# Optimization experiments

Measured on AMD Instinct MI355X. Metric: run time of the kernel, lower is better.

Reference implementation:

```python
import jax, jax.numpy as jnp
import numpy as np

# Dimensions (match init_kwargs / input_specs)
N, F, E = 50000, 256, 200000   # nodes, in-features, edges
H, C = 4, 128                  # heads, per-head channels (hidden_dim)
G, NC = 256, 10                # graphs in batch, num_classes
EPS = 1e-16                    # PyG softmax denominator epsilon


def _lin(key, fin, fout):
    kw, kb = jax.random.split(key)
    W = jax.random.normal(kw, (fin, fout), jnp.float32) / np.float32(np.sqrt(fin))
    b = jax.random.normal(kb, (fout,), jnp.float32) * 0.01
    return W, b


def setup_inputs() -> dict:
    key = jax.random.key(0)
    ks = jax.random.split(key, 16)
    x = jax.random.normal(ks[0], (N, F), jnp.float32)
    edge_index = jax.random.randint(ks[1], (2, E), 0, N)
    batch = jnp.sort(jax.random.randint(ks[2], (N,), 0, G))
    d = {"x": x, "edge_index": edge_index, "batch": batch}
    # layer1: in=F, out=H*C (concat=True); layer2: in=H*C, out=C (concat=False, skip -> C)
    d["Wq1"], d["bq1"] = _lin(ks[3], F, H * C)
    d["Wk1"], d["bk1"] = _lin(ks[4], F, H * C)
    d["Wv1"], d["bv1"] = _lin(ks[5], F, H * C)
    d["Ws1"], d["bs1"] = _lin(ks[6], F, H * C)
    d["Wq2"], d["bq2"] = _lin(ks[7], H * C, H * C)
    d["Wk2"], d["bk2"] = _lin(ks[8], H * C, H * C)
    d["Wv2"], d["bv2"] = _lin(ks[9], H * C, H * C)
    d["Ws2"], d["bs2"] = _lin(ks[10], H * C, C)
    d["Wfc"], d["bfc"] = _lin(ks[11], C, NC)
    return d


def _tconv(x, src, dst, Wq, bq, Wk, bk, Wv, bv, Ws, bs, concat):
    """PyG TransformerConv (root_weight=True, beta=False), eval mode (no dropout)."""
    n = x.shape[0]
    q = (x @ Wq + bq).reshape(n, H, C)
    k = (x @ Wk + bk).reshape(n, H, C)
    v = (x @ Wv + bv).reshape(n, H, C)
    # per-edge scores: query from dst node i, key/value from src node j
    alpha = jnp.einsum('ehc,ehc->eh', q[dst], k[src]) / jnp.float32(np.sqrt(C))  # [E,H]
    m = jax.ops.segment_max(alpha, dst, num_segments=n)          # [N,H]
    e = jnp.exp(alpha - m[dst])                                  # [E,H]
    s = jax.ops.segment_sum(e, dst, num_segments=n)              # [N,H]
    a = e / (s[dst] + EPS)                                       # segment softmax over dst
    msg = jax.ops.segment_sum(a[:, :, None] * v[src], dst, num_segments=n)  # [N,H,C]
    out = msg.reshape(n, H * C) if concat else msg.mean(axis=1)
    return out + x @ Ws + bs  # root/skip connection


def reference(x, edge_index, batch,
              Wq1, bq1, Wk1, bk1, Wv1, bv1, Ws1, bs1,
              Wq2, bq2, Wk2, bk2, Wv2, bv2, Ws2, bs2,
              Wfc, bfc):
    src, dst = edge_index[0], edge_index[1]
    h = jax.nn.elu(_tconv(x, src, dst, Wq1, bq1, Wk1, bk1, Wv1, bv1, Ws1, bs1, True))
    # dropout is identity in eval mode
    h = jax.nn.elu(_tconv(h, src, dst, Wq2, bq2, Wk2, bk2, Wv2, bv2, Ws2, bs2, False))
    cnt = jax.ops.segment_sum(jnp.ones((h.shape[0],), h.dtype), batch, num_segments=G)
    pooled = jax.ops.segment_sum(h, batch, num_segments=G) / jnp.maximum(cnt, 1.0)[:, None]
    return jax.nn.log_softmax(pooled @ Wfc + bfc, axis=1)  # [G, NC]
```

## Files before the change

### kernel.cpp

```cpp
#include <hip/hip_runtime.h>
#include <math.h>
#include <stdint.h>

#define N_NODES 50000
#define FEAT    256
#define EDGES   200000
#define HEADS   4
#define CH      128
#define HID     512
#define NGRAPH  256
#define NCLS    10

typedef unsigned short ushort_t;
typedef unsigned int uint_t;
typedef __attribute__((ext_vector_type(8))) short bf16x8;
typedef __attribute__((ext_vector_type(4))) float f32x4;
typedef __attribute__((ext_vector_type(2))) float f32x2;

__device__ __forceinline__ ushort_t f2bf(float f) {
  uint_t u = __float_as_uint(f);
  u += 0x7FFF + ((u >> 16) & 1);
  return (ushort_t)(u >> 16);
}
__device__ __forceinline__ float bf2f(ushort_t h) {
  return __uint_as_float(((uint_t)h) << 16);
}
__device__ __forceinline__ float elu1(float x) {
  return x > 0.f ? x : __expf(x) - 1.f;
}
__device__ __forceinline__ float fastrcp(float x) {
  return __builtin_amdgcn_rcpf(x);
}
__device__ __forceinline__ void unpack8(uint4 w, float* f) {
  f[0] = bf2f((ushort_t)w.x); f[1] = bf2f((ushort_t)(w.x >> 16));
  f[2] = bf2f((ushort_t)w.y); f[3] = bf2f((ushort_t)(w.y >> 16));
  f[4] = bf2f((ushort_t)w.z); f[5] = bf2f((ushort_t)(w.z >> 16));
  f[6] = bf2f((ushort_t)w.w); f[7] = bf2f((ushort_t)(w.w >> 16));
}
__device__ __forceinline__ void unpack8_fp8(uint2 w, float* f) {
  f32x2 a = __builtin_amdgcn_cvt_pk_f32_fp8((int)w.x, false);
  f32x2 b = __builtin_amdgcn_cvt_pk_f32_fp8((int)w.x, true);
  f32x2 c = __builtin_amdgcn_cvt_pk_f32_fp8((int)w.y, false);
  f32x2 d = __builtin_amdgcn_cvt_pk_f32_fp8((int)w.y, true);
  f[0] = a[0]; f[1] = a[1]; f[2] = b[0]; f[3] = b[1];
  f[4] = c[0]; f[5] = c[1]; f[6] = d[0]; f[7] = d[1];
}
__device__ __forceinline__ uint_t pack4_fp8(float f0, float f1, float f2, float f3) {
  int v = __builtin_amdgcn_cvt_pk_fp8_f32(f0, f1, 0, false);
  v = __builtin_amdgcn_cvt_pk_fp8_f32(f2, f3, v, true);
  return (uint_t)v;
}


__global__ __launch_bounds__(256) void gemm_bt(
    const ushort_t* __restrict__ A, const ushort_t* __restrict__ Bt,
    const float* __restrict__ bias, char* __restrict__ Cb,
    char* __restrict__ Cb2, int M, int K, int nct, int mode) {
  __shared__ __align__(16) ushort_t smem[24576];
  const int tid = threadIdx.x;
  const int lane = tid & 63, wave = tid >> 6;
  const int wr = wave >> 1, wc = wave & 1;

  int b = blockIdx.x;
  int per = nct << 3;
  int grp = b / per;
  int rem = b - grp * per;
  int rloc = rem & 7;
  int ct = rem >> 3;
  const int rowBase = (grp * 8 + rloc) * 128;
  const int colBase = ct * 128;
  if (rowBase >= M) return;

  const int s0 = tid, s1 = tid + 256;
  const int rl0 = s0 >> 2, cg0 = (s0 & 3) ^ ((rl0 >> 1) & 3);
  const int rl1 = s1 >> 2, cg1 = (s1 & 3) ^ ((rl1 >> 1) & 3);
  int ra0 = rowBase + rl0; ra0 = ra0 < M ? ra0 : M - 1;
  int ra1 = rowBase + rl1; ra1 = ra1 < M ? ra1 : M - 1;
  const ushort_t* pa0 = A + (size_t)ra0 * K + cg0 * 8;
  const ushort_t* pa1 = A + (size_t)ra1 * K + cg1 * 8;
  const ushort_t* pb0 = Bt + (size_t)(colBase + rl0) * K + cg0 * 8;
  const ushort_t* pb1 = Bt + (size_t)(colBase + rl1) * K + cg1 * 8;
  const int dA0 = s0 * 8, dA1 = s1 * 8;
  const int dB0 = 4096 + s0 * 8, dB1 = 4096 + s1 * 8;

#define GLL(gp, loff)  __builtin_amdgcn_global_load_lds( \
      (const __attribute__((address_space(1))) uint_t*)(gp), \
      (__attribute__((address_space(3))) uint_t*)(smem + (loff)), 16, 0, 0)

  const int nt = K >> 5;
  GLL(pa0, dA0);            GLL(pa1, dA1);
  GLL(pb0, dB0);            GLL(pb1, dB1);
  GLL(pa0 + 32, 8192 + dA0); GLL(pa1 + 32, 8192 + dA1);
  GLL(pb0 + 32, 8192 + dB0); GLL(pb1 + 32, 8192 + dB1);
  pa0 += 64; pa1 += 64; pb0 += 64; pb1 += 64;

  const int fr = lane & 15, c0 = lane >> 4;
  const int pswz = (c0 ^ ((fr >> 1) & 3)) * 8;
  const int aOff = (wr * 64 + fr) * 32 + pswz;
  const int bOff = 4096 + (wc * 64 + fr) * 32 + pswz;

  f32x4 acc[4][4] = {};
  asm volatile("s_waitcnt vmcnt(4)" ::: "memory");
  __builtin_amdgcn_s_barrier();
  __builtin_amdgcn_sched_barrier(0);

  int cur = 0, nxt = 2;
  for (int t = 0; t < nt; ++t) {
    const ushort_t* bufc = smem + cur * 8192;
    const bool pf = (t + 2) < nt;
    bf16x8 af[4], bfr[4];
    af[0] = *(const bf16x8*)(bufc + aOff);
#pragma unroll
    for (int j = 0; j < 4; ++j) bfr[j] = *(const bf16x8*)(bufc + bOff + j * 512);
#pragma unroll
    for (int i = 1; i < 4; ++i) af[i] = *(const bf16x8*)(bufc + aOff + i * 512);
    if (pf) {
      int lo = nxt * 8192;
      GLL(pa0, lo + dA0); GLL(pa1, lo + dA1);
      GLL(pb0, lo + dB0); GLL(pb1, lo + dB1);
      pa0 += 32; pa1 += 32; pb0 += 32; pb1 += 32;
    }
#pragma unroll
    for (int i = 0; i < 4; ++i)
#pragma unroll
      for (int j = 0; j < 4; ++j)
        acc[i][j] = __builtin_amdgcn_mfma_f32_16x16x32_bf16(af[i], bfr[j], acc[i][j], 0, 0, 0);
    asm volatile("s_waitcnt lgkmcnt(0)" ::: "memory");
    if (pf)                asm volatile("s_waitcnt vmcnt(4)" ::: "memory");
    else if (t + 1 < nt)   asm volatile("s_waitcnt vmcnt(0)" ::: "memory");
    __builtin_amdgcn_s_barrier();
    __builtin_amdgcn_sched_barrier(0);
    cur = cur == 2 ? 0 : cur + 1;
    nxt = nxt == 2 ? 0 : nxt + 1;
  }
#undef GLL

  char* obase; int ostride, koff, isfp8;
  if (mode == 1) {
    int H = colBase >> 9, sel = (colBase >> 7) & 3;
    if (sel == 0)      { obase = Cb;  ostride = 2304; koff = H * 256; isfp8 = 0; }
    else if (sel == 3) { obase = Cb2; ostride = 1024; koff = H * 256; isfp8 = 0; }
    else { obase = Cb; ostride = 2304;
           koff = 1024 + H * 256 + (sel == 2 ? 8 : 0); isfp8 = 1; }
  } else {
    obase = Cb; ostride = 2304;
    if (colBase == 768) { koff = 2048; isfp8 = 0; }
    else {
      int n2 = (colBase < 768) ? colBase : colBase - 896;
      int hb = (colBase < 768) ? 0 : 2;
      int hh = hb + n2 / 384, r = n2 % 384, sel = r >> 7;
      if (sel == 0) { koff = hh * 256; isfp8 = 0; }
      else          { koff = 1024 + hh * 256 + (sel == 2 ? 8 : 0); isfp8 = 1; }
    }
  }

  ushort_t* wbuf = smem + wave * 2048;
  const int rq = lane >> 4, fc = lane & 15;
  float bv[4];
#pragma unroll
  for (int j = 0; j < 4; ++j) bv[j] = bias[colBase + wc * 64 + j * 16 + fc];
#pragma unroll
  for (int h = 0; h < 2; ++h) {
#pragma unroll
    for (int ii = 0; ii < 2; ++ii) {
      int i = h * 2 + ii;
#pragma unroll
      for (int j = 0; j < 4; ++j)
#pragma unroll
        for (int r = 0; r < 4; ++r) {
          int rl = ii * 16 + rq * 4 + r;
          int cl = j * 16 + fc;
          int cs = cl ^ (rq << 4);
          wbuf[rl * 64 + cs] = f2bf(acc[i][j][r] + bv[j]);
        }
    }
    int ci = lane & 7;
    int rbase = lane >> 3;
#pragma unroll
    for (int rg = 0; rg < 4; ++rg) {
      int rr = rg * 8 + rbase;
      int rowg = rowBase + wr * 64 + h * 32 + rr;
      int cg = ci ^ (((rr >> 2) & 3) << 1);
      uint4 val = *(const uint4*)(wbuf + rr * 64 + (ci << 3));
      if (rowg < M) {
        char* dstRow = obase + (size_t)rowg * ostride + koff;
        if (!isfp8) {
          *(uint4*)(dstRow + (wc * 64 + cg * 8) * 2) = val;
        } else {
          float f[8];
          f[0] = bf2f((ushort_t)val.x); f[1] = bf2f((ushort_t)(val.x >> 16));
          f[2] = bf2f((ushort_t)val.y); f[3] = bf2f((ushort_t)(val.y >> 16));
          f[4] = bf2f((ushort_t)val.z); f[5] = bf2f((ushort_t)(val.z >> 16));
          f[6] = bf2f((ushort_t)val.w); f[7] = bf2f((ushort_t)(val.w >> 16));
          uint2 o;
          o.x = pack4_fp8(f[0], f[1], f[2], f[3]);
          o.y = pack4_fp8(f[4], f[5], f[6], f[7]);
          *(uint2*)(dstRow + ((wc * 8 + cg) << 4)) = o;
        }
      }
    }
  }
}

#define L1_W   (2048 * FEAT)
#define L2_W   (1664 * HID)
#define T1     512
#define T2     832
#define NB_CVT  12500
#define NB_TP   (T1 + T2)
#define NB_BIAS 15
#define NB_ZERO 196

__global__ __launch_bounds__(256) void prep_all(
    const float* __restrict__ x, ushort_t* __restrict__ xb,
    const float* __restrict__ Wq1, const float* __restrict__ Wk1,
    const float* __restrict__ Wv1, const float* __restrict__ Ws1,
    const float* __restrict__ Wq2, const float* __restrict__ Wk2,
    const float* __restrict__ Wv2, const float* __restrict__ Ws2,
    const float* __restrict__ bq1, const float* __restrict__ bk1,
    const float* __restrict__ bv1, const float* __restrict__ bs1,
    const float* __restrict__ bq2, const float* __restrict__ bk2,
    const float* __restrict__ bv2, const float* __restrict__ bs2,
    ushort_t* __restrict__ W1t, ushort_t* __restrict__ W2t,
    float* __restrict__ Bh1, float* __restrict__ Bh2,
    int* __restrict__ deg, int* __restrict__ counter,
    int* __restrict__ gstart, int* __restrict__ gend) {
  __shared__ float tile[32][33];
  int blk = blockIdx.x;
  if (blk < NB_CVT) {
    int i = blk * 256 + threadIdx.x;
    float4 f = *(const float4*)(x + (size_t)i * 4);
    uint_t lo = (uint_t)f2bf(f.x) | ((uint_t)f2bf(f.y) << 16);
    uint_t hi = (uint_t)f2bf(f.z) | ((uint_t)f2bf(f.w) << 16);
    ((uint2*)xb)[i] = make_uint2(lo, hi);
    return;
  }
  blk -= NB_CVT;
  if (blk < NB_TP) {
    int t = blk;
    const float* W; int ldw, c0, n0, k0, ldk; ushort_t* dst;
    if (t < T1) {
      int nb = t >> 3, kb = t & 7;
      n0 = nb * 32; k0 = kb * 32; ldk = FEAT; dst = W1t;
      int p = n0 >> 10, n1 = n0 & 1023, hh = n1 >> 9, sel = (n1 >> 7) & 3;
      c0 = (2 * p + hh) * CH + (n1 & (CH - 1));
      W = sel == 0 ? Wq1 : sel == 1 ? Wk1 : sel == 2 ? Wv1 : Ws1;
      ldw = HID;
    } else {
      t -= T1;
      int nb = t >> 4, kb = t & 15;
      n0 = nb * 32; k0 = kb * 32; ldk = HID; dst = W2t;
      if (n0 < 768 || n0 >= 896) {
        int n2 = (n0 < 768) ? n0 : n0 - 896;
        int hb = (n0 < 768) ? 0 : 2;
        int hh = hb + n2 / 384, r = n2 % 384, sel = r >> 7;
        c0 = hh * CH + (r & (CH - 1));
        W = sel == 0 ? Wq2 : sel == 1 ? Wk2 : Wv2;
        ldw = HID;
      } else {
        c0 = n0 - 768; W = Ws2; ldw = CH;
      }
    }
    int col = threadIdx.x & 31, rw = threadIdx.x >> 5;
#pragma unroll
    for (int ph = 0; ph < 4; ++ph) {
      int kk = rw + ph * 8;
      tile[kk][col] = W[(size_t)(k0 + kk) * ldw + c0 + col];
    }
    __syncthreads();
#pragma unroll
    for (int ph = 0; ph < 4; ++ph) {
      int dn = rw + ph * 8;
      dst[(size_t)(n0 + dn) * ldk + k0 + col] = f2bf(tile[col][dn]);
    }
    return;
  }
  blk -= NB_TP;
  if (blk < NB_BIAS) {
    int n = blk * 256 + threadIdx.x;
    if (n < 2048) {
      int p = n >> 10, n1 = n & 1023, hh = n1 >> 9, sel = (n1 >> 7) & 3;
      int c = (2 * p + hh) * CH + (n1 & (CH - 1));
      const float* bb = sel == 0 ? bq1 : sel == 1 ? bk1 : sel == 2 ? bv1 : bs1;
      Bh1[n] = bb[c];
    } else if (n < 2048 + 1664) {
      int n2 = n - 2048;
      if (n2 < 768 || n2 >= 896) {
        int nn = (n2 < 768) ? n2 : n2 - 896;
        int hb = (n2 < 768) ? 0 : 2;
        int hh = hb + nn / 384, r = nn % 384, sel = r >> 7;
        int c = hh * CH + (r & (CH - 1));
        const float* bb = sel == 0 ? bq2 : sel == 1 ? bk2 : bv2;
        Bh2[n2] = bb[c];
      } else {
        Bh2[n2] = bs2[n2 - 768];
      }
    }
    return;
  }
  blk -= NB_BIAS;
  {
    int i = blk * 256 + threadIdx.x;
    if (i < N_NODES) deg[i] = 0;
    if (i < NGRAPH) { gstart[i] = 0; gend[i] = 0; }
    if (i == 0) counter[0] = 0;
  }
}

__global__ void hist_bounds_kernel(const int* __restrict__ dst, int* __restrict__ deg,
                                   const int* __restrict__ batch,
                                   int* __restrict__ gstart, int* __restrict__ gend) {
  int t = blockIdx.x * blockDim.x + threadIdx.x;
  if (t < EDGES) atomicAdd(&deg[dst[t]], 1);
  if (t < N_NODES) {
    int b = batch[t];
    if (t == 0 || batch[t - 1] != b) gstart[b] = t;
    if (t == N_NODES - 1 || batch[t + 1] != b) gend[b] = t + 1;
  }
}

__global__ void alloc_kernel(const int* __restrict__ deg, int* __restrict__ counter,
                             int* __restrict__ start, int* __restrict__ cursor) {
  int i = blockIdx.x * blockDim.x + threadIdx.x;
  int lane = threadIdx.x & 63;
  int v = (i < N_NODES) ? deg[i] : 0;
  int sum = v;
#pragma unroll
  for (int off = 1; off < 64; off <<= 1) {
    int t = __shfl_up(sum, off);
    if (lane >= off) sum += t;
  }
  int excl = sum - v;
  int waveTot = __shfl(sum, 63);
  int base = 0;
  if (lane == 63) base = atomicAdd(counter, waveTot);
  base = __shfl(base, 63);
  if (i < N_NODES) {
    start[i] = base + excl;
    cursor[i] = base + excl;
  }
}

__global__ void scatter_kernel(const int* __restrict__ src, const int* __restrict__ dst,
                               int* __restrict__ cursor, int* __restrict__ csr) {
  int e = blockIdx.x * blockDim.x + threadIdx.x;
  if (e < EDGES) {
    int pos = atomicAdd(&cursor[dst[e]], 1);
    csr[pos] = src[e];
  }
}

#define INV_SQRT_CH 0.08838834764831845f

__global__ __launch_bounds__(256) void attn1_kernel(
    const char* __restrict__ BIG, const int* __restrict__ start,
    const int* __restrict__ deg, const int* __restrict__ csr,
    ushort_t* __restrict__ H1b) {
  int wave = threadIdx.x >> 6, lane = threadIdx.x & 63;
  int li = lane & 15, g = lane >> 4;
  int i = blockIdx.x * 4 + wave;
  if (i >= N_NODES) return;
  int beg = start[i], end = beg + deg[i];
  const int kvoff = 1024 + g * 256 + li * 16;
  float q[8];
  unpack8(*(const uint4*)(BIG + (size_t)i * 2304 + g * 256 + li * 16), q);
  float s = 0.f, a[8] = {};
  if (beg < end) {
    int j = csr[beg];
    uint4 kv = *(const uint4*)(BIG + (size_t)j * 2304 + kvoff);
    for (int e = beg; e < end; ++e) {
      int en = e + 1 < end ? e + 1 : e;
      int jn = csr[en];
      uint4 kvn = *(const uint4*)(BIG + (size_t)jn * 2304 + kvoff);
      float kf[8];
      unpack8_fp8(make_uint2(kv.x, kv.y), kf);
      float pd = q[0]*kf[0]+q[1]*kf[1]+q[2]*kf[2]+q[3]*kf[3]+
                 q[4]*kf[4]+q[5]*kf[5]+q[6]*kf[6]+q[7]*kf[7];
      pd += __shfl_xor(pd, 1);
      pd += __shfl_xor(pd, 2);
      pd += __shfl_xor(pd, 4);
      pd += __shfl_xor(pd, 8);
      float w = __expf(pd * INV_SQRT_CH);
      float vf[8];
      unpack8_fp8(make_uint2(kv.z, kv.w), vf);
      s += w;
#pragma unroll
      for (int c = 0; c < 8; ++c) a[c] = fmaf(w, vf[c], a[c]);
      kv = kvn;
    }
  }
  float inv = fastrcp(s + 1e-16f);
  ushort_t* op8 = H1b + (size_t)i * HID + g * CH + li * 8;
  float sk[8];
  unpack8(*(const uint4*)op8, sk);
  uint4 ow;
  uint_t* op = (uint_t*)&ow;
#pragma unroll
  for (int c = 0; c < 4; ++c) {
    float o0 = elu1(a[2 * c] * inv + sk[2 * c]);
    float o1 = elu1(a[2 * c + 1] * inv + sk[2 * c + 1]);
    op[c] = (uint_t)f2bf(o0) | ((uint_t)f2bf(o1) << 16);
  }
  *(uint4*)op8 = ow;
}

__global__ __launch_bounds__(256) void attn2_kernel(
    const char* __restrict__ BIG, const int* __restrict__ start,
    const int* __restrict__ deg, const int* __restrict__ csr,
    ushort_t* __restrict__ POut) {
  int wave = threadIdx.x >> 6, lane = threadIdx.x & 63;
  int li = lane & 15, g = lane >> 4;
  int i = blockIdx.x * 4 + wave;
  if (i >= N_NODES) return;
  int beg = start[i], end = beg + deg[i];
  const int kvoff = 1024 + g * 256 + li * 16;
  float q[8];
  unpack8(*(const uint4*)(BIG + (size_t)i * 2304 + g * 256 + li * 16), q);
  float s = 0.f, a[8] = {};
  if (beg < end) {
    int j = csr[beg];
    uint4 kv = *(const uint4*)(BIG + (size_t)j * 2304 + kvoff);
    for (int e = beg; e < end; ++e) {
      int en = e + 1 < end ? e + 1 : e;
      int jn = csr[en];
      uint4 kvn = *(const uint4*)(BIG + (size_t)jn * 2304 + kvoff);
      float kf[8];
      unpack8_fp8(make_uint2(kv.x, kv.y), kf);
      float pd = q[0]*kf[0]+q[1]*kf[1]+q[2]*kf[2]+q[3]*kf[3]+
                 q[4]*kf[4]+q[5]*kf[5]+q[6]*kf[6]+q[7]*kf[7];
      pd += __shfl_xor(pd, 1);
      pd += __shfl_xor(pd, 2);
      pd += __shfl_xor(pd, 4);
      pd += __shfl_xor(pd, 8);
      float w = __expf(pd * INV_SQRT_CH);
      float vf[8];
      unpack8_fp8(make_uint2(kv.z, kv.w), vf);
      s += w;
#pragma unroll
      for (int c = 0; c < 8; ++c) a[c] = fmaf(w, vf[c], a[c]);
      kv = kvn;
    }
  }
  float inv = 0.25f * fastrcp(s + 1e-16f);
  float o[8];
#pragma unroll
  for (int c = 0; c < 8; ++c) o[c] = a[c] * inv;
#pragma unroll
  for (int ox = 16; ox <= 32; ox <<= 1)
#pragma unroll
    for (int c = 0; c < 8; ++c) o[c] += __shfl_xor(o[c], ox);
  if (g != 0) return;
  uint4 ow;
  uint_t* op = (uint_t*)&ow;
#pragma unroll
  for (int c = 0; c < 4; ++c)
    op[c] = (uint_t)f2bf(o[2 * c]) | ((uint_t)f2bf(o[2 * c + 1]) << 16);
  *(uint4*)(POut + (size_t)i * CH + li * 8) = ow;
}

__global__ __launch_bounds__(256) void pool_cls(
    const ushort_t* __restrict__ POut, const char* __restrict__ BIG,
    const int* __restrict__ gstart, const int* __restrict__ gend,
    const float* __restrict__ Wfc, const float* __restrict__ bfc,
    float* __restrict__ out) {
  int g = blockIdx.x;
  int t = threadIdx.x;
  int c = t & (CH - 1), rr = t >> 7;
  int s0 = gstart[g], e0 = gend[g];
  float sum = 0.f;
  for (int i = s0 + rr; i < e0; i += 2) {
    float sk = bf2f(*(const ushort_t*)(BIG + (size_t)i * 2304 + 2048 + c * 2));
    float m0 = bf2f(POut[(size_t)i * CH + c]);
    sum += elu1(sk + m0);
  }
  __shared__ float sh[256];
  __shared__ float p[CH];
  __shared__ float red[CH];
  __shared__ float logits[NCLS];
  sh[t] = sum;
  __syncthreads();
  if (t < CH) {
    float cnt = fmaxf((float)(e0 - s0), 1.f);
    p[t] = (sh[t] + sh[t + CH]) / cnt;
  }
  for (int cc = 0; cc < NCLS; ++cc) {
    __syncthreads();
    if (t < CH) red[t] = p[t] * Wfc[t * NCLS + cc];
    __syncthreads();
    for (int off = 64; off > 0; off >>= 1) {
      if (t < off) red[t] += red[t + off];
      __syncthreads();
    }
    if (t == 0) logits[cc] = red[0] + bfc[cc];
  }
  __syncthreads();
  if (t == 0) {
    float mx = -INFINITY;
    for (int cc = 0; cc < NCLS; ++cc) mx = fmaxf(mx, logits[cc]);
    float se = 0.f;
    for (int cc = 0; cc < NCLS; ++cc) se += expf(logits[cc] - mx);
    float ls = mx + logf(se);
    for (int cc = 0; cc < NCLS; ++cc) out[g * NCLS + cc] = logits[cc] - ls;
  }
}

extern "C" void kernel_launch(void* const* d_in, const int* in_sizes, int n_in,
                              void* d_out, int out_size, void* d_ws, size_t ws_size,
                              hipStream_t stream) {
  const float* x    = (const float*)d_in[0];
  const int*   ei   = (const int*)d_in[1];
  const int*   batch= (const int*)d_in[2];
  const float* Wq1 = (const float*)d_in[3];  const float* bq1 = (const float*)d_in[4];
  const float* Wk1 = (const float*)d_in[5];  const float* bk1 = (const float*)d_in[6];
  const float* Wv1 = (const float*)d_in[7];  const float* bv1 = (const float*)d_in[8];
  const float* Ws1 = (const float*)d_in[9];  const float* bs1 = (const float*)d_in[10];
  const float* Wq2 = (const float*)d_in[11]; const float* bq2 = (const float*)d_in[12];
  const float* Wk2 = (const float*)d_in[13]; const float* bk2 = (const float*)d_in[14];
  const float* Wv2 = (const float*)d_in[15]; const float* bv2 = (const float*)d_in[16];
  const float* Ws2 = (const float*)d_in[17]; const float* bs2 = (const float*)d_in[18];
  const float* Wfc = (const float*)d_in[19]; const float* bfc = (const float*)d_in[20];
  float* out = (float*)d_out;

  ushort_t* xb     = (ushort_t*)d_ws;
  ushort_t* POut   = (ushort_t*)d_ws;
  char*     BIG    = (char*)(xb + (size_t)N_NODES * FEAT);
  ushort_t* H1b    = (ushort_t*)(BIG + (size_t)N_NODES * 2304);
  ushort_t* W1t    = H1b + (size_t)N_NODES * HID;
  float*    Bh1    = (float*)(W1t + L1_W);
  ushort_t* W2t    = (ushort_t*)(Bh1 + 2048);
  float*    Bh2    = (float*)(W2t + L2_W);
  int* deg    = (int*)(Bh2 + 1664);
  int* start  = deg + N_NODES;
  int* cursor = start + N_NODES;
  int* csr    = cursor + N_NODES;
  int* gstart = csr + EDGES;
  int* gend   = gstart + NGRAPH;
  int* counter= gend + NGRAPH;

  const int* srcp = ei;
  const int* dstp = ei + EDGES;

  prep_all<<<NB_CVT + NB_TP + NB_BIAS + NB_ZERO, 256, 0, stream>>>(
      x, xb, Wq1, Wk1, Wv1, Ws1, Wq2, Wk2, Wv2, Ws2,
      bq1, bk1, bv1, bs1, bq2, bk2, bv2, bs2,
      W1t, W2t, Bh1, Bh2, deg, counter, gstart, gend);
  hist_bounds_kernel<<<(EDGES + 255) / 256, 256, 0, stream>>>(dstp, deg, batch, gstart, gend);
  alloc_kernel<<<(N_NODES + 255) / 256, 256, 0, stream>>>(deg, counter, start, cursor);
  scatter_kernel<<<(EDGES + 255) / 256, 256, 0, stream>>>(srcp, dstp, cursor, csr);

  const int ga = (N_NODES + 3) / 4;

  gemm_bt<<<49 * 8 * 16, 256, 0, stream>>>(
      xb, W1t, Bh1, BIG, (char*)H1b, N_NODES, FEAT, 16, 1);
  attn1_kernel<<<ga, 256, 0, stream>>>(BIG, start, deg, csr, H1b);

  gemm_bt<<<49 * 8 * 13, 256, 0, stream>>>(
      H1b, W2t, Bh2, BIG, (char*)H1b, N_NODES, HID, 13, 2);
  attn2_kernel<<<ga, 256, 0, stream>>>(BIG, start, deg, csr, POut);

  pool_cls<<<NGRAPH, 256, 0, stream>>>(POut, BIG, gstart, gend, Wfc, bfc, out);
}
```

Measured before the change: 472.6 us.

## Unroll attention edge loops by two and split pooling across chunked blocks

The attention kernels now process two edges per iteration with separate accumulators and two gathers in flight, which adds memory-level parallelism to the latency-bound neighbor gathers. Attn1 also loads the skip values before the loop rather than after it. The pooling+classifier kernel is split into a chunked partial-sum kernel (256x8 blocks with float atomics into a zeroed buffer) and a small final classifier kernel. This raises parallelism in pooling but adds one launch and makes the float summation order nondeterministic.

```diff
diff --git a/kernel.cpp b/kernel.cpp
--- a/kernel.cpp
+++ b/kernel.cpp
@@ -224,7 +224,8 @@
     ushort_t* __restrict__ W1t, ushort_t* __restrict__ W2t,
     float* __restrict__ Bh1, float* __restrict__ Bh2,
     int* __restrict__ deg, int* __restrict__ counter,
-    int* __restrict__ gstart, int* __restrict__ gend) {
+    int* __restrict__ gstart, int* __restrict__ gend,
+    float* __restrict__ pooled) {
   __shared__ float tile[32][33];
   int blk = blockIdx.x;
   if (blk < NB_CVT) {
@@ -303,6 +304,7 @@
     int i = blk * 256 + threadIdx.x;
     if (i < N_NODES) deg[i] = 0;
     if (i < NGRAPH) { gstart[i] = 0; gend[i] = 0; }
+    if (i < NGRAPH * CH) pooled[i] = 0.f;
     if (i == 0) counter[0] = 0;
   }
 }
@@ -364,41 +366,67 @@
   const int kvoff = 1024 + g * 256 + li * 16;
   float q[8];
   unpack8(*(const uint4*)(BIG + (size_t)i * 2304 + g * 256 + li * 16), q);
-  float s = 0.f, a[8] = {};
-  if (beg < end) {
-    int j = csr[beg];
-    uint4 kv = *(const uint4*)(BIG + (size_t)j * 2304 + kvoff);
-    for (int e = beg; e < end; ++e) {
-      int en = e + 1 < end ? e + 1 : e;
-      int jn = csr[en];
-      uint4 kvn = *(const uint4*)(BIG + (size_t)jn * 2304 + kvoff);
-      float kf[8];
-      unpack8_fp8(make_uint2(kv.x, kv.y), kf);
-      float pd = q[0]*kf[0]+q[1]*kf[1]+q[2]*kf[2]+q[3]*kf[3]+
-                 q[4]*kf[4]+q[5]*kf[5]+q[6]*kf[6]+q[7]*kf[7];
-      pd += __shfl_xor(pd, 1);
-      pd += __shfl_xor(pd, 2);
-      pd += __shfl_xor(pd, 4);
-      pd += __shfl_xor(pd, 8);
-      float w = __expf(pd * INV_SQRT_CH);
-      float vf[8];
-      unpack8_fp8(make_uint2(kv.z, kv.w), vf);
-      s += w;
-#pragma unroll
-      for (int c = 0; c < 8; ++c) a[c] = fmaf(w, vf[c], a[c]);
-      kv = kvn;
-    }
-  }
+  ushort_t* op8 = H1b + (size_t)i * HID + g * CH + li * 8;
+  uint4 skw = *(const uint4*)op8;
+  float sA = 0.f, sB = 0.f, aA[8] = {}, aB[8] = {};
+  uint4 kv0 = make_uint4(0, 0, 0, 0), kv1 = make_uint4(0, 0, 0, 0);
+  int e = beg;
+  if (e < end)     kv0 = *(const uint4*)(BIG + (size_t)csr[e] * 2304 + kvoff);
+  if (e + 1 < end) kv1 = *(const uint4*)(BIG + (size_t)csr[e + 1] * 2304 + kvoff);
+  for (; e + 2 <= end; e += 2) {
+    int i2 = e + 2 < end ? e + 2 : end - 1;
+    int i3 = e + 3 < end ? e + 3 : end - 1;
+    uint4 kn0 = *(const uint4*)(BIG + (size_t)csr[i2] * 2304 + kvoff);
+    uint4 kn1 = *(const uint4*)(BIG + (size_t)csr[i3] * 2304 + kvoff);
+    float kf[8];
+    unpack8_fp8(make_uint2(kv0.x, kv0.y), kf);
+    float p0 = q[0]*kf[0]+q[1]*kf[1]+q[2]*kf[2]+q[3]*kf[3]+
+               q[4]*kf[4]+q[5]*kf[5]+q[6]*kf[6]+q[7]*kf[7];
+    unpack8_fp8(make_uint2(kv1.x, kv1.y), kf);
+    float p1 = q[0]*kf[0]+q[1]*kf[1]+q[2]*kf[2]+q[3]*kf[3]+
+               q[4]*kf[4]+q[5]*kf[5]+q[6]*kf[6]+q[7]*kf[7];
+#pragma unroll
+    for (int ox = 1; ox <= 8; ox <<= 1) {
+      p0 += __shfl_xor(p0, ox);
+      p1 += __shfl_xor(p1, ox);
+    }
+    float w0 = __expf(p0 * INV_SQRT_CH);
+    float w1 = __expf(p1 * INV_SQRT_CH);
+    float vf[8];
+    unpack8_fp8(make_uint2(kv0.z, kv0.w), vf);
+    sA += w0;
+#pragma unroll
+    for (int c = 0; c < 8; ++c) aA[c] = fmaf(w0, vf[c], aA[c]);
+    unpack8_fp8(make_uint2(kv1.z, kv1.w), vf);
+    sB += w1;
+#pragma unroll
+    for (int c = 0; c < 8; ++c) aB[c] = fmaf(w1, vf[c], aB[c]);
+    kv0 = kn0; kv1 = kn1;
+  }
+  if (e < end) {
+    float kf[8];
+    unpack8_fp8(make_uint2(kv0.x, kv0.y), kf);
+    float p0 = q[0]*kf[0]+q[1]*kf[1]+q[2]*kf[2]+q[3]*kf[3]+
+               q[4]*kf[4]+q[5]*kf[5]+q[6]*kf[6]+q[7]*kf[7];
+#pragma unroll
+    for (int ox = 1; ox <= 8; ox <<= 1) p0 += __shfl_xor(p0, ox);
+    float w0 = __expf(p0 * INV_SQRT_CH);
+    float vf[8];
+    unpack8_fp8(make_uint2(kv0.z, kv0.w), vf);
+    sA += w0;
+#pragma unroll
+    for (int c = 0; c < 8; ++c) aA[c] = fmaf(w0, vf[c], aA[c]);
+  }
+  float s = sA + sB;
   float inv = fastrcp(s + 1e-16f);
-  ushort_t* op8 = H1b + (size_t)i * HID + g * CH + li * 8;
   float sk[8];
-  unpack8(*(const uint4*)op8, sk);
+  unpack8(skw, sk);
   uint4 ow;
   uint_t* op = (uint_t*)&ow;
 #pragma unroll
   for (int c = 0; c < 4; ++c) {
-    float o0 = elu1(a[2 * c] * inv + sk[2 * c]);
-    float o1 = elu1(a[2 * c + 1] * inv + sk[2 * c + 1]);
+    float o0 = elu1((aA[2 * c] + aB[2 * c]) * inv + sk[2 * c]);
+    float o1 = elu1((aA[2 * c + 1] + aB[2 * c + 1]) * inv + sk[2 * c + 1]);
     op[c] = (uint_t)f2bf(o0) | ((uint_t)f2bf(o1) << 16);
   }
   *(uint4*)op8 = ow;
@@ -416,35 +444,60 @@
   const int kvoff = 1024 + g * 256 + li * 16;
   float q[8];
   unpack8(*(const uint4*)(BIG + (size_t)i * 2304 + g * 256 + li * 16), q);
-  float s = 0.f, a[8] = {};
-  if (beg < end) {
-    int j = csr[beg];
-    uint4 kv = *(const uint4*)(BIG + (size_t)j * 2304 + kvoff);
-    for (int e = beg; e < end; ++e) {
-      int en = e + 1 < end ? e + 1 : e;
-      int jn = csr[en];
-      uint4 kvn = *(const uint4*)(BIG + (size_t)jn * 2304 + kvoff);
-      float kf[8];
-      unpack8_fp8(make_uint2(kv.x, kv.y), kf);
-      float pd = q[0]*kf[0]+q[1]*kf[1]+q[2]*kf[2]+q[3]*kf[3]+
-                 q[4]*kf[4]+q[5]*kf[5]+q[6]*kf[6]+q[7]*kf[7];
-      pd += __shfl_xor(pd, 1);
-      pd += __shfl_xor(pd, 2);
-      pd += __shfl_xor(pd, 4);
-      pd += __shfl_xor(pd, 8);
-      float w = __expf(pd * INV_SQRT_CH);
-      float vf[8];
-      unpack8_fp8(make_uint2(kv.z, kv.w), vf);
-      s += w;
-#pragma unroll
-      for (int c = 0; c < 8; ++c) a[c] = fmaf(w, vf[c], a[c]);
-      kv = kvn;
-    }
-  }
+  float sA = 0.f, sB = 0.f, aA[8] = {}, aB[8] = {};
+  uint4 kv0 = make_uint4(0, 0, 0, 0), kv1 = make_uint4(0, 0, 0, 0);
+  int e = beg;
+  if (e < end)     kv0 = *(const uint4*)(BIG + (size_t)csr[e] * 2304 + kvoff);
+  if (e + 1 < end) kv1 = *(const uint4*)(BIG + (size_t)csr[e + 1] * 2304 + kvoff);
+  for (; e + 2 <= end; e += 2) {
+    int i2 = e + 2 < end ? e + 2 : end - 1;
+    int i3 = e + 3 < end ? e + 3 : end - 1;
+    uint4 kn0 = *(const uint4*)(BIG + (size_t)csr[i2] * 2304 + kvoff);
+    uint4 kn1 = *(const uint4*)(BIG + (size_t)csr[i3] * 2304 + kvoff);
+    float kf[8];
+    unpack8_fp8(make_uint2(kv0.x, kv0.y), kf);
+    float p0 = q[0]*kf[0]+q[1]*kf[1]+q[2]*kf[2]+q[3]*kf[3]+
+               q[4]*kf[4]+q[5]*kf[5]+q[6]*kf[6]+q[7]*kf[7];
+    unpack8_fp8(make_uint2(kv1.x, kv1.y), kf);
+    float p1 = q[0]*kf[0]+q[1]*kf[1]+q[2]*kf[2]+q[3]*kf[3]+
+               q[4]*kf[4]+q[5]*kf[5]+q[6]*kf[6]+q[7]*kf[7];
+#pragma unroll
+    for (int ox = 1; ox <= 8; ox <<= 1) {
+      p0 += __shfl_xor(p0, ox);
+      p1 += __shfl_xor(p1, ox);
+    }
+    float w0 = __expf(p0 * INV_SQRT_CH);
+    float w1 = __expf(p1 * INV_SQRT_CH);
+    float vf[8];
+    unpack8_fp8(make_uint2(kv0.z, kv0.w), vf);
+    sA += w0;
+#pragma unroll
+    for (int c = 0; c < 8; ++c) aA[c] = fmaf(w0, vf[c], aA[c]);
+    unpack8_fp8(make_uint2(kv1.z, kv1.w), vf);
+    sB += w1;
+#pragma unroll
+    for (int c = 0; c < 8; ++c) aB[c] = fmaf(w1, vf[c], aB[c]);
+    kv0 = kn0; kv1 = kn1;
+  }
+  if (e < end) {
+    float kf[8];
+    unpack8_fp8(make_uint2(kv0.x, kv0.y), kf);
+    float p0 = q[0]*kf[0]+q[1]*kf[1]+q[2]*kf[2]+q[3]*kf[3]+
+               q[4]*kf[4]+q[5]*kf[5]+q[6]*kf[6]+q[7]*kf[7];
+#pragma unroll
+    for (int ox = 1; ox <= 8; ox <<= 1) p0 += __shfl_xor(p0, ox);
+    float w0 = __expf(p0 * INV_SQRT_CH);
+    float vf[8];
+    unpack8_fp8(make_uint2(kv0.z, kv0.w), vf);
+    sA += w0;
+#pragma unroll
+    for (int c = 0; c < 8; ++c) aA[c] = fmaf(w0, vf[c], aA[c]);
+  }
+  float s = sA + sB;
   float inv = 0.25f * fastrcp(s + 1e-16f);
   float o[8];
 #pragma unroll
-  for (int c = 0; c < 8; ++c) o[c] = a[c] * inv;
+  for (int c = 0; c < 8; ++c) o[c] = (aA[c] + aB[c]) * inv;
 #pragma unroll
   for (int ox = 16; ox <= 32; ox <<= 1)
 #pragma unroll
@@ -458,50 +511,48 @@
   *(uint4*)(POut + (size_t)i * CH + li * 8) = ow;
 }
 
-__global__ __launch_bounds__(256) void pool_cls(
+__global__ __launch_bounds__(256) void pool_partial(
     const ushort_t* __restrict__ POut, const char* __restrict__ BIG,
     const int* __restrict__ gstart, const int* __restrict__ gend,
-    const float* __restrict__ Wfc, const float* __restrict__ bfc,
-    float* __restrict__ out) {
-  int g = blockIdx.x;
+    float* __restrict__ pooled) {
+  int g = blockIdx.x, chunk = blockIdx.y;
   int t = threadIdx.x;
   int c = t & (CH - 1), rr = t >> 7;
   int s0 = gstart[g], e0 = gend[g];
   float sum = 0.f;
-  for (int i = s0 + rr; i < e0; i += 2) {
+  for (int i = s0 + chunk * 2 + rr; i < e0; i += 16) {
     float sk = bf2f(*(const ushort_t*)(BIG + (size_t)i * 2304 + 2048 + c * 2));
     float m0 = bf2f(POut[(size_t)i * CH + c]);
     sum += elu1(sk + m0);
   }
-  __shared__ float sh[256];
-  __shared__ float p[CH];
-  __shared__ float red[CH];
-  __shared__ float logits[NCLS];
-  sh[t] = sum;
-  __syncthreads();
-  if (t < CH) {
-    float cnt = fmaxf((float)(e0 - s0), 1.f);
-    p[t] = (sh[t] + sh[t + CH]) / cnt;
-  }
-  for (int cc = 0; cc < NCLS; ++cc) {
-    __syncthreads();
-    if (t < CH) red[t] = p[t] * Wfc[t * NCLS + cc];
-    __syncthreads();
-    for (int off = 64; off > 0; off >>= 1) {
-      if (t < off) red[t] += red[t + off];
-      __syncthreads();
-    }
-    if (t == 0) logits[cc] = red[0] + bfc[cc];
-  }
-  __syncthreads();
-  if (t == 0) {
-    float mx = -INFINITY;
-    for (int cc = 0; cc < NCLS; ++cc) mx = fmaxf(mx, logits[cc]);
-    float se = 0.f;
-    for (int cc = 0; cc < NCLS; ++cc) se += expf(logits[cc] - mx);
-    float ls = mx + logf(se);
-    for (int cc = 0; cc < NCLS; ++cc) out[g * NCLS + cc] = logits[cc] - ls;
-  }
+  atomicAdd(&pooled[g * CH + c], sum);
+}
+
+__global__ __launch_bounds__(256) void cls_final(
+    const float* __restrict__ pooled, const int* __restrict__ gstart,
+    const int* __restrict__ gend, const float* __restrict__ Wfc,
+    const float* __restrict__ bfc, float* __restrict__ out) {
+  int g = blockIdx.x * blockDim.x + threadIdx.x;
+  if (g >= NGRAPH) return;
+  float inv = 1.f / fmaxf((float)(gend[g] - gstart[g]), 1.f);
+  float logits[NCLS];
+#pragma unroll
+  for (int cc = 0; cc < NCLS; ++cc) logits[cc] = bfc[cc];
+  for (int c = 0; c < CH; ++c) {
+    float p = pooled[g * CH + c] * inv;
+#pragma unroll
+    for (int cc = 0; cc < NCLS; ++cc)
+      logits[cc] = fmaf(p, Wfc[c * NCLS + cc], logits[cc]);
+  }
+  float mx = -INFINITY;
+#pragma unroll
+  for (int cc = 0; cc < NCLS; ++cc) mx = fmaxf(mx, logits[cc]);
+  float se = 0.f;
+#pragma unroll
+  for (int cc = 0; cc < NCLS; ++cc) se += expf(logits[cc] - mx);
+  float ls = mx + logf(se);
+#pragma unroll
+  for (int cc = 0; cc < NCLS; ++cc) out[g * NCLS + cc] = logits[cc] - ls;
 }
 
 extern "C" void kernel_launch(void* const* d_in, const int* in_sizes, int n_in,
@@ -536,6 +587,7 @@
   int* gstart = csr + EDGES;
   int* gend   = gstart + NGRAPH;
   int* counter= gend + NGRAPH;
+  float* pooled = (float*)(counter + 1);
 
   const int* srcp = ei;
   const int* dstp = ei + EDGES;
@@ -543,7 +595,7 @@
   prep_all<<<NB_CVT + NB_TP + NB_BIAS + NB_ZERO, 256, 0, stream>>>(
       x, xb, Wq1, Wk1, Wv1, Ws1, Wq2, Wk2, Wv2, Ws2,
       bq1, bk1, bv1, bs1, bq2, bk2, bv2, bs2,
-      W1t, W2t, Bh1, Bh2, deg, counter, gstart, gend);
+      W1t, W2t, Bh1, Bh2, deg, counter, gstart, gend, pooled);
   hist_bounds_kernel<<<(EDGES + 255) / 256, 256, 0, stream>>>(dstp, deg, batch, gstart, gend);
   alloc_kernel<<<(N_NODES + 255) / 256, 256, 0, stream>>>(deg, counter, start, cursor);
   scatter_kernel<<<(EDGES + 255) / 256, 256, 0, stream>>>(srcp, dstp, cursor, csr);
@@ -558,5 +610,6 @@
       H1b, W2t, Bh2, BIG, (char*)H1b, N_NODES, HID, 13, 2);
   attn2_kernel<<<ga, 256, 0, stream>>>(BIG, start, deg, csr, POut);
 
-  pool_cls<<<NGRAPH, 256, 0, stream>>>(POut, BIG, gstart, gend, Wfc, bfc, out);
-}
+  pool_partial<<<dim3(NGRAPH, 8), 256, 0, stream>>>(POut, BIG, gstart, gend, pooled);
+  cls_final<<<1, 256, 0, stream>>>(pooled, gstart, gend, Wfc, bfc, out);
+}
```

Result: faster. 450.8 us (-4.6%).
